# Kernel optimization log

Hardware: AMD Instinct MI355X
Metric: run time of the kernel (lower is better)

Reference implementation:

```python
import jax, jax.numpy as jnp
import numpy as np

B, IN, OUT, G, K = 8192, 2048, 2048, 5, 3
EPS = 1e-8


def b_spline_basis(x, grid, k=K):
    # x: [B, in], grid: [in, G]
    Gn = grid.shape[1]
    diff = x[:, :, None] - grid[None, :, :]                      # [B, in, G]
    basis = ((diff >= 0) & (diff < 1)).astype(x.dtype)           # order-0 indicator
    for order in range(1, k + 1):
        js = np.arange(Gn - order)
        i2 = np.minimum(js + order, Gn - 1)       # clamp of original OOB index
        i3 = np.minimum(js + order + 1, Gn - 1)   # clamp of original OOB index
        prev = basis
        # note: original uses (diff[:,:,j] - grid[:,j]) = x - 2*grid[:,j]; kept faithfully
        t1 = (diff[:, :, js] - grid[:, js]) / (grid[:, i2] - grid[:, js] + EPS) * prev[:, :, js]
        t2 = (grid[:, i3] - diff[:, :, js]) / (grid[:, i3] - grid[:, js + 1] + EPS) * prev[:, :, js + 1]
        basis = basis.at[:, :, js].set(t1 + t2)
    return basis


def setup_inputs() -> dict:
    key = jax.random.key(0)
    k1, k2, k3, k4, k5 = jax.random.split(key, 5)
    bound = 1.0 / np.sqrt(IN)
    x = jax.random.normal(k1, (B, IN), dtype=jnp.float32)
    base_weight = jax.random.uniform(k2, (OUT, IN), dtype=jnp.float32, minval=-bound, maxval=bound)
    base_bias = jax.random.uniform(k3, (OUT,), dtype=jnp.float32, minval=-bound, maxval=bound)
    spline_weight = jax.random.uniform(k4, (OUT, IN, G), dtype=jnp.float32, minval=-0.1, maxval=0.1)
    grid = jax.random.uniform(k5, (IN, G), dtype=jnp.float32, minval=-1.0, maxval=1.0)
    return {"x": x, "base_weight": base_weight, "base_bias": base_bias,
            "spline_weight": spline_weight, "grid": grid}


def reference(x, base_weight, base_bias, spline_weight, grid):
    base_output = x @ base_weight.T + base_bias                   # [B, out]
    spline_basis = b_spline_basis(x, grid, K)                     # [B, in, G]
    spline_output = jnp.einsum('big,oig->bo', spline_basis, spline_weight)
    return base_output + spline_output
```

## Files before the change

### kernel.cpp

```cpp
#include <hip/hip_runtime.h>
#include <hip/hip_bf16.h>

#define EPS 1e-8f

constexpr int B_   = 8192;
constexpr int IN_  = 2048;
constexpr int OUT_ = 2048;
constexpr int KA_  = IN_ * 6;
constexpr int NT_  = KA_ / 64;

typedef __bf16 bf16x8 __attribute__((ext_vector_type(8)));
typedef float  f32x4  __attribute__((ext_vector_type(4)));

__device__ __forceinline__ ushort f2bf(float f) {
    union { float f; uint u; } v; v.f = f;
    uint u = v.u;
    uint r = u + 0x7fffu + ((u >> 16) & 1u);
    return (ushort)(r >> 16);
}

__device__ __forceinline__ void gload16(const void* g, void* l) {
    __builtin_amdgcn_global_load_lds(
        (const __attribute__((address_space(1))) void*)g,
        (__attribute__((address_space(3))) void*)l,
        16, 0, 0);
}

__global__ __launch_bounds__(256) void stage_a(const float* __restrict__ x,
                                               const float* __restrict__ grid,
                                               ushort* __restrict__ A) {
    __shared__ __attribute__((aligned(16))) ushort pack[1536];
    const int tid = threadIdx.x;
    const int b0  = blockIdx.x * 16;
    const int i0  = blockIdx.y * 256;
    const int i   = i0 + tid;

    float g[5];
#pragma unroll
    for (int j = 0; j < 5; ++j) g[j] = grid[i * 5 + j];

    float r1[9], r2[9];
    {
        int t = 0;
#pragma unroll
        for (int o = 1; o <= 3; ++o) {
#pragma unroll
            for (int j = 0; j < 5 - o; ++j) {
                int i2 = min(j + o, 4);
                int i3 = min(j + o + 1, 4);
                r1[t] = 1.0f / (g[i2] - g[j] + EPS);
                r2[t] = 1.0f / (g[i3] - g[j + 1] + EPS);
                ++t;
            }
        }
    }

    for (int r = 0; r < 16; ++r) {
        const int b = b0 + r;
        float xv = x[(size_t)b * IN_ + i];
        float diff[5], bas[5];
#pragma unroll
        for (int j = 0; j < 5; ++j) {
            diff[j] = xv - g[j];
            bas[j]  = (diff[j] >= 0.0f && diff[j] < 1.0f) ? 1.0f : 0.0f;
        }
        int t = 0;
#pragma unroll
        for (int o = 1; o <= 3; ++o) {
            float nb[4];
#pragma unroll
            for (int j = 0; j < 5 - o; ++j) {
                int i3 = min(j + o + 1, 4);
                float t1 = (diff[j] - g[j]) * r1[t] * bas[j];
                float t2 = (g[i3] - diff[j]) * r2[t] * bas[j + 1];
                nb[j] = t1 + t2;
                ++t;
            }
#pragma unroll
            for (int j = 0; j < 5 - o; ++j) bas[j] = nb[j];
        }

        pack[tid * 6 + 0] = f2bf(xv);
#pragma unroll
        for (int j = 0; j < 5; ++j) pack[tid * 6 + 1 + j] = f2bf(bas[j]);
        __syncthreads();
        {
            const uint* ps = (const uint*)pack;
            uint* pd = (uint*)(A + (size_t)b * KA_ + (size_t)i0 * 6);
#pragma unroll
            for (int j = 0; j < 3; ++j) pd[tid + j * 256] = ps[tid + j * 256];
        }
        __syncthreads();
    }
}

__global__ __launch_bounds__(256) void stage_w(const float* __restrict__ bw,
                                               const float* __restrict__ sw,
                                               ushort* __restrict__ W) {
    __shared__ __attribute__((aligned(16))) float  ssh[1280];
    __shared__ __attribute__((aligned(16))) ushort wsh[1536];
    const int tid = threadIdx.x;
    const int o   = blockIdx.x;
    const int i0  = blockIdx.y * 256;

    const float* sp = sw + ((size_t)o * IN_ + i0) * 5;
    for (int j = tid; j < 1280; j += 256) ssh[j] = sp[j];
    float bwv = bw[(size_t)o * IN_ + i0 + tid];
    __syncthreads();

    wsh[tid * 6] = f2bf(bwv);
#pragma unroll
    for (int j = 0; j < 5; ++j) wsh[tid * 6 + 1 + j] = f2bf(ssh[tid * 5 + j]);
    __syncthreads();

    const uint* ps = (const uint*)wsh;
    uint* pd = (uint*)(W + (size_t)o * KA_ + (size_t)i0 * 6);
#pragma unroll
    for (int j = 0; j < 3; ++j) pd[tid + j * 256] = ps[tid + j * 256];
}

__global__ __launch_bounds__(512, 2) void gemm_kan8(const ushort* __restrict__ A,
                                                    const ushort* __restrict__ W,
                                                    const float* __restrict__ bias,
                                                    float* __restrict__ out) {
    __shared__ __attribute__((aligned(16))) char lds[2][2][32768];

    const int tid  = threadIdx.x;
    const int lane = tid & 63;
    const int wave = tid >> 6;
    const int wr   = wave >> 2;
    const int wc   = wave & 3;

    uint bid = blockIdx.x;
    uint swz = (bid & 7u) * 32u + (bid >> 3);
    const int bm = (int)(swz >> 3);
    const int bn = (int)(swz & 7u);

    const uint lhi16 = ((uint)lane >> 4) * 16u;
    const uint swx   = ((uint)lane & 7u) << 4;
    uint aro[8], wro[4];
#pragma unroll
    for (int m = 0; m < 8; ++m) aro[m] = (uint)(wr * 128 + m * 16 + (lane & 15)) * 128u;
#pragma unroll
    for (int n = 0; n < 4; ++n) wro[n] = (uint)(wc * 64 + n * 16 + (lane & 15)) * 128u;

    const uint srow0 = (uint)wave * 8u + ((uint)lane >> 3);
    const uint srow1 = srow0 + 64u;
    const uint gcol  = (((uint)lane & 7u) ^ (((uint)lane >> 3) & 7u)) * 8u;
    const ushort* pA0 = A + (size_t)bm * 256 * KA_ + (size_t)srow0 * KA_ + gcol;
    const ushort* pA1 = A + (size_t)bm * 256 * KA_ + (size_t)srow1 * KA_ + gcol;
    const ushort* pW0 = W + (size_t)bn * 256 * KA_ + (size_t)srow0 * KA_ + gcol;
    const ushort* pW1 = W + (size_t)bn * 256 * KA_ + (size_t)srow1 * KA_ + gcol;
    const uint c0off = (uint)wave * 1024u;
    const uint c1off = c0off + 8192u;

    f32x4 acc[8][4];
#pragma unroll
    for (int m = 0; m < 8; ++m)
#pragma unroll
        for (int n = 0; n < 4; ++n)
            acc[m][n] = (f32x4){0.f, 0.f, 0.f, 0.f};

#define DSR(base, ro, kh) (*(const bf16x8*)((base) + (ro) + (((kh) * 64u + lhi16) ^ swx)))

#define STAGE(s, mat, h, kk, PT0, PT1) do {                                   \
        uint kc_ = (uint)((kk) < NT_ ? (kk) : 0);                             \
        size_t go_ = (size_t)(h) * 128 * KA_ + (size_t)kc_ * 64;              \
        gload16(PT0 + go_, &lds[s][mat][(h) * 16384 + c0off]);                \
        gload16(PT1 + go_, &lds[s][mat][(h) * 16384 + c1off]);                \
    } while (0)

#define RDA(dst, base, mb) do {                                               \
        _Pragma("unroll") for (int m_ = 0; m_ < 4; ++m_) {                    \
            dst[m_][0] = DSR(base, aro[(mb) + m_], 0);                        \
            dst[m_][1] = DSR(base, aro[(mb) + m_], 1); } } while (0)

#define RDB(dst, base, nb) do {                                               \
        _Pragma("unroll") for (int n_ = 0; n_ < 2; ++n_) {                    \
            dst[n_][0] = DSR(base, wro[(nb) + n_], 0);                        \
            dst[n_][1] = DSR(base, wro[(nb) + n_], 1); } } while (0)

#define MIDBAR() do { __builtin_amdgcn_s_barrier();                           \
        asm volatile("s_waitcnt lgkmcnt(0)" ::: "memory");                    \
        __builtin_amdgcn_sched_barrier(0); } while (0)

#define MFMAQ(AF, BF, MB, NB) do {                                            \
        __builtin_amdgcn_s_setprio(1);                                        \
        _Pragma("unroll") for (int m_ = 0; m_ < 4; ++m_)                      \
        _Pragma("unroll") for (int n_ = 0; n_ < 2; ++n_) {                    \
            acc[(MB)+m_][(NB)+n_] = __builtin_amdgcn_mfma_f32_16x16x32_bf16(  \
                AF[m_][0], BF[n_][0], acc[(MB)+m_][(NB)+n_], 0, 0, 0);        \
            acc[(MB)+m_][(NB)+n_] = __builtin_amdgcn_mfma_f32_16x16x32_bf16(  \
                AF[m_][1], BF[n_][1], acc[(MB)+m_][(NB)+n_], 0, 0, 0);        \
        }                                                                     \
        __builtin_amdgcn_s_setprio(0);                                        \
        __builtin_amdgcn_s_barrier(); } while (0)

    const char* As0 = lds[0][0]; const char* Ws0 = lds[0][1];
    const char* As1 = lds[1][0]; const char* Ws1 = lds[1][1];

    STAGE(0, 0, 0, 0, pA0, pA1);
    STAGE(0, 0, 1, 0, pA0, pA1);
    STAGE(0, 1, 0, 0, pW0, pW1);
    STAGE(0, 1, 1, 0, pW0, pW1);
    STAGE(1, 1, 0, 1, pW0, pW1);
    STAGE(1, 1, 1, 1, pW0, pW1);
    asm volatile("s_waitcnt vmcnt(4)" ::: "memory");
    __builtin_amdgcn_s_barrier();

    bf16x8 a0[4][2], a1[4][2], b0[2][2], b1[2][2];

    for (int it = 0; it < NT_ / 2; ++it) {
        const int t1 = 2 * it + 1;
        RDA(a0, As0, 0); RDB(b0, Ws0, 0);
        STAGE(1, 0, 0, t1, pA0, pA1);
        MIDBAR(); MFMAQ(a0, b0, 0, 0);
        RDB(b1, Ws0, 2);
        STAGE(1, 0, 1, t1, pA0, pA1);
        MIDBAR(); MFMAQ(a0, b1, 0, 2);
        RDA(a1, As0, 4);
        STAGE(0, 1, 0, t1 + 1, pW0, pW1);
        MIDBAR(); MFMAQ(a1, b0, 4, 0);
        STAGE(0, 1, 1, t1 + 1, pW0, pW1);
        asm volatile("s_waitcnt vmcnt(4)" ::: "memory");
        MIDBAR(); MFMAQ(a1, b1, 4, 2);
        RDA(a0, As1, 0); RDB(b0, Ws1, 0);
        STAGE(0, 0, 0, t1 + 1, pA0, pA1);
        MIDBAR(); MFMAQ(a0, b0, 0, 0);
        RDB(b1, Ws1, 2);
        STAGE(0, 0, 1, t1 + 1, pA0, pA1);
        MIDBAR(); MFMAQ(a0, b1, 0, 2);
        RDA(a1, As1, 4);
        STAGE(1, 1, 0, t1 + 2, pW0, pW1);
        MIDBAR(); MFMAQ(a1, b0, 4, 0);
        STAGE(1, 1, 1, t1 + 2, pW0, pW1);
        asm volatile("s_waitcnt vmcnt(4)" ::: "memory");
        MIDBAR(); MFMAQ(a1, b1, 4, 2);
    }

    const int orow0 = bm * 256 + wr * 128;
    const int ocol0 = bn * 256 + wc * 64;
#pragma unroll
    for (int n = 0; n < 4; ++n) {
        int c = ocol0 + n * 16 + (lane & 15);
        float bv = bias[c];
#pragma unroll
        for (int m = 0; m < 8; ++m) {
            int r0 = orow0 + m * 16 + ((lane >> 4) << 2);
#pragma unroll
            for (int j = 0; j < 4; ++j)
                out[(size_t)(r0 + j) * OUT_ + c] = acc[m][n][j] + bv;
        }
    }
#undef DSR
#undef STAGE
#undef RDA
#undef RDB
#undef MIDBAR
#undef MFMAQ
}

__global__ __launch_bounds__(256) void kan_fallback(const float* __restrict__ x,
                                                    const float* __restrict__ bw,
                                                    const float* __restrict__ bb,
                                                    const float* __restrict__ sw,
                                                    const float* __restrict__ grid,
                                                    float* __restrict__ out) {
    __shared__ float ash[16 * 384];
    const int tid = threadIdx.x;
    const int o   = blockIdx.x * 256 + tid;
    const int b0  = blockIdx.y * 16;
    float acc[16];
#pragma unroll
    for (int r = 0; r < 16; ++r) acc[r] = 0.0f;

    for (int ic = 0; ic < IN_; ic += 64) {
        __syncthreads();
        for (int p = tid; p < 1024; p += 256) {
            int r = p >> 6, ii = p & 63;
            int i = ic + ii;
            float xv = x[(size_t)(b0 + r) * IN_ + i];
            float g[5];
#pragma unroll
            for (int j = 0; j < 5; ++j) g[j] = grid[i * 5 + j];
            float diff[5], bas[5];
#pragma unroll
            for (int j = 0; j < 5; ++j) {
                diff[j] = xv - g[j];
                bas[j]  = (diff[j] >= 0.0f && diff[j] < 1.0f) ? 1.0f : 0.0f;
            }
#pragma unroll
            for (int oo = 1; oo <= 3; ++oo) {
                float nb[4];
#pragma unroll
                for (int j = 0; j < 5 - oo; ++j) {
                    int i2 = min(j + oo, 4);
                    int i3 = min(j + oo + 1, 4);
                    nb[j] = (diff[j] - g[j]) / (g[i2] - g[j] + EPS) * bas[j]
                          + (g[i3] - diff[j]) / (g[i3] - g[j + 1] + EPS) * bas[j + 1];
                }
#pragma unroll
                for (int j = 0; j < 5 - oo; ++j) bas[j] = nb[j];
            }
            float* ap = &ash[r * 384 + ii * 6];
            ap[0] = xv;
#pragma unroll
            for (int j = 0; j < 5; ++j) ap[1 + j] = bas[j];
        }
        __syncthreads();
        for (int ii = 0; ii < 64; ++ii) {
            int i = ic + ii;
            float w0 = bw[(size_t)o * IN_ + i];
            const float* swp = sw + ((size_t)o * IN_ + i) * 5;
            float w1 = swp[0], w2 = swp[1], w3 = swp[2], w4 = swp[3], w5 = swp[4];
#pragma unroll
            for (int r = 0; r < 16; ++r) {
                const float* a = &ash[r * 384 + ii * 6];
                acc[r] += a[0] * w0 + a[1] * w1 + a[2] * w2
                        + a[3] * w3 + a[4] * w4 + a[5] * w5;
            }
        }
    }
    float bv = bb[o];
#pragma unroll
    for (int r = 0; r < 16; ++r)
        out[(size_t)(b0 + r) * OUT_ + o] = acc[r] + bv;
}

extern "C" void kernel_launch(void* const* d_in, const int* in_sizes, int n_in,
                              void* d_out, int out_size, void* d_ws, size_t ws_size,
                              hipStream_t stream) {
    (void)in_sizes; (void)n_in; (void)out_size;
    const float* x    = (const float*)d_in[0];
    const float* bw   = (const float*)d_in[1];
    const float* bb   = (const float*)d_in[2];
    const float* sw   = (const float*)d_in[3];
    const float* grid = (const float*)d_in[4];
    float* out = (float*)d_out;

    const size_t needA = (size_t)B_ * KA_ * sizeof(ushort);
    const size_t needW = (size_t)OUT_ * KA_ * sizeof(ushort);

    if (ws_size >= needA + needW) {
        ushort* A = (ushort*)d_ws;
        ushort* W = A + (size_t)B_ * KA_;
        stage_a<<<dim3(B_ / 16, IN_ / 256), 256, 0, stream>>>(x, grid, A);
        stage_w<<<dim3(OUT_, IN_ / 256), 256, 0, stream>>>(bw, sw, W);
        gemm_kan8<<<dim3(256), 512, 0, stream>>>(A, W, bb, out);
    } else {
        kan_fallback<<<dim3(OUT_ / 256, B_ / 16), 256, 0, stream>>>(x, bw, bb, sw, grid, out);
    }
}
```

Measured before the change: 422.4 us.

## Switch GEMM inner loop from 16x16x32 to 32x32x16 MFMA tiles

Replaces the 16x16x32 bf16 MFMA micro-tiles with 32x32x16 instructions. Each wave now covers its 128x64 output with 4x2 accumulator tiles of 16 floats, and the LDS read pattern and swizzle offsets are reworked to match the 32-row fragment layout. B fragments for all four k-subslices are loaded once per tile stage and A is reloaded per k-subslice. The epilogue is remapped to the 32x32 accumulator register layout. The intent is fewer LDS reads per flop and higher MFMA throughput, at the cost of different register pressure and a different LDS access pattern.

```diff
diff --git a/kernel.cpp b/kernel.cpp
--- a/kernel.cpp
+++ b/kernel.cpp
@@ -10,7 +10,7 @@
 constexpr int NT_  = KA_ / 64;
 
 typedef __bf16 bf16x8 __attribute__((ext_vector_type(8)));
-typedef float  f32x4  __attribute__((ext_vector_type(4)));
+typedef float  f32x16 __attribute__((ext_vector_type(16)));
 
 __device__ __forceinline__ ushort f2bf(float f) {
     union { float f; uint u; } v; v.f = f;
@@ -136,13 +136,13 @@
     const int bm = (int)(swz >> 3);
     const int bn = (int)(swz & 7u);
 
-    const uint lhi16 = ((uint)lane >> 4) * 16u;
-    const uint swx   = ((uint)lane & 7u) << 4;
-    uint aro[8], wro[4];
-#pragma unroll
-    for (int m = 0; m < 8; ++m) aro[m] = (uint)(wr * 128 + m * 16 + (lane & 15)) * 128u;
-#pragma unroll
-    for (int n = 0; n < 4; ++n) wro[n] = (uint)(wc * 64 + n * 16 + (lane & 15)) * 128u;
+    const uint l5   = ((uint)lane >> 5) * 16u;
+    const uint swx  = ((uint)lane & 7u) << 4;
+    uint aro[4], wro[2];
+#pragma unroll
+    for (int m = 0; m < 4; ++m) aro[m] = (uint)(wr * 128 + m * 32 + (lane & 31)) * 128u;
+#pragma unroll
+    for (int n = 0; n < 2; ++n) wro[n] = (uint)(wc * 64 + n * 32 + (lane & 31)) * 128u;
 
     const uint srow0 = (uint)wave * 8u + ((uint)lane >> 3);
     const uint srow1 = srow0 + 64u;
@@ -154,14 +154,14 @@
     const uint c0off = (uint)wave * 1024u;
     const uint c1off = c0off + 8192u;
 
-    f32x4 acc[8][4];
-#pragma unroll
-    for (int m = 0; m < 8; ++m)
-#pragma unroll
-        for (int n = 0; n < 4; ++n)
-            acc[m][n] = (f32x4){0.f, 0.f, 0.f, 0.f};
-
-#define DSR(base, ro, kh) (*(const bf16x8*)((base) + (ro) + (((kh) * 64u + lhi16) ^ swx)))
+    f32x16 acc[4][2];
+#pragma unroll
+    for (int m = 0; m < 4; ++m)
+#pragma unroll
+        for (int n = 0; n < 2; ++n)
+            acc[m][n] = (f32x16)(0.0f);
+
+#define DSR32(base, ro, kh) (*(const bf16x8*)((base) + (ro) + (((kh) * 32u + l5) ^ swx)))
 
 #define STAGE(s, mat, h, kk, PT0, PT1) do {                                   \
         uint kc_ = (uint)((kk) < NT_ ? (kk) : 0);                             \
@@ -170,31 +170,28 @@
         gload16(PT1 + go_, &lds[s][mat][(h) * 16384 + c1off]);                \
     } while (0)
 
-#define RDA(dst, base, mb) do {                                               \
-        _Pragma("unroll") for (int m_ = 0; m_ < 4; ++m_) {                    \
-            dst[m_][0] = DSR(base, aro[(mb) + m_], 0);                        \
-            dst[m_][1] = DSR(base, aro[(mb) + m_], 1); } } while (0)
-
-#define RDB(dst, base, nb) do {                                               \
-        _Pragma("unroll") for (int n_ = 0; n_ < 2; ++n_) {                    \
-            dst[n_][0] = DSR(base, wro[(nb) + n_], 0);                        \
-            dst[n_][1] = DSR(base, wro[(nb) + n_], 1); } } while (0)
+#define RDA32(dst, base, kh) do {                                             \
+        _Pragma("unroll") for (int m_ = 0; m_ < 4; ++m_)                      \
+            dst[m_] = DSR32(base, aro[m_], kh); } while (0)
+
+#define RDB32(dst, base) do {                                                 \
+        _Pragma("unroll") for (int n_ = 0; n_ < 2; ++n_)                      \
+        _Pragma("unroll") for (int k_ = 0; k_ < 4; ++k_)                      \
+            dst[n_][k_] = DSR32(base, wro[n_], k_); } while (0)
 
 #define MIDBAR() do { __builtin_amdgcn_s_barrier();                           \
         asm volatile("s_waitcnt lgkmcnt(0)" ::: "memory");                    \
         __builtin_amdgcn_sched_barrier(0); } while (0)
 
-#define MFMAQ(AF, BF, MB, NB) do {                                            \
+#define MFMA8(AF, BF, KH) do {                                                \
         __builtin_amdgcn_s_setprio(1);                                        \
         _Pragma("unroll") for (int m_ = 0; m_ < 4; ++m_)                      \
-        _Pragma("unroll") for (int n_ = 0; n_ < 2; ++n_) {                    \
-            acc[(MB)+m_][(NB)+n_] = __builtin_amdgcn_mfma_f32_16x16x32_bf16(  \
-                AF[m_][0], BF[n_][0], acc[(MB)+m_][(NB)+n_], 0, 0, 0);        \
-            acc[(MB)+m_][(NB)+n_] = __builtin_amdgcn_mfma_f32_16x16x32_bf16(  \
-                AF[m_][1], BF[n_][1], acc[(MB)+m_][(NB)+n_], 0, 0, 0);        \
-        }                                                                     \
-        __builtin_amdgcn_s_setprio(0);                                        \
-        __builtin_amdgcn_s_barrier(); } while (0)
+        _Pragma("unroll") for (int n_ = 0; n_ < 2; ++n_)                      \
+            acc[m_][n_] = __builtin_amdgcn_mfma_f32_32x32x16_bf16(            \
+                AF[m_], BF[n_][KH], acc[m_][n_], 0, 0, 0);                    \
+        __builtin_amdgcn_s_setprio(0); } while (0)
+
+#define ENDBAR() __builtin_amdgcn_s_barrier()
 
     const char* As0 = lds[0][0]; const char* Ws0 = lds[0][1];
     const char* As1 = lds[1][0]; const char* Ws1 = lds[1][1];
@@ -208,56 +205,61 @@
     asm volatile("s_waitcnt vmcnt(4)" ::: "memory");
     __builtin_amdgcn_s_barrier();
 
-    bf16x8 a0[4][2], a1[4][2], b0[2][2], b1[2][2];
+    bf16x8 a[4], b[2][4];
 
     for (int it = 0; it < NT_ / 2; ++it) {
         const int t1 = 2 * it + 1;
-        RDA(a0, As0, 0); RDB(b0, Ws0, 0);
+        RDA32(a, As0, 0); RDB32(b, Ws0);
         STAGE(1, 0, 0, t1, pA0, pA1);
-        MIDBAR(); MFMAQ(a0, b0, 0, 0);
-        RDB(b1, Ws0, 2);
+        MIDBAR(); MFMA8(a, b, 0); ENDBAR();
+        RDA32(a, As0, 1);
         STAGE(1, 0, 1, t1, pA0, pA1);
-        MIDBAR(); MFMAQ(a0, b1, 0, 2);
-        RDA(a1, As0, 4);
+        MIDBAR(); MFMA8(a, b, 1); ENDBAR();
+        RDA32(a, As0, 2);
         STAGE(0, 1, 0, t1 + 1, pW0, pW1);
-        MIDBAR(); MFMAQ(a1, b0, 4, 0);
+        MIDBAR(); MFMA8(a, b, 2); ENDBAR();
+        RDA32(a, As0, 3);
         STAGE(0, 1, 1, t1 + 1, pW0, pW1);
         asm volatile("s_waitcnt vmcnt(4)" ::: "memory");
-        MIDBAR(); MFMAQ(a1, b1, 4, 2);
-        RDA(a0, As1, 0); RDB(b0, Ws1, 0);
+        MIDBAR(); MFMA8(a, b, 3); ENDBAR();
+        RDA32(a, As1, 0); RDB32(b, Ws1);
         STAGE(0, 0, 0, t1 + 1, pA0, pA1);
-        MIDBAR(); MFMAQ(a0, b0, 0, 0);
-        RDB(b1, Ws1, 2);
+        MIDBAR(); MFMA8(a, b, 0); ENDBAR();
+        RDA32(a, As1, 1);
         STAGE(0, 0, 1, t1 + 1, pA0, pA1);
-        MIDBAR(); MFMAQ(a0, b1, 0, 2);
-        RDA(a1, As1, 4);
+        MIDBAR(); MFMA8(a, b, 1); ENDBAR();
+        RDA32(a, As1, 2);
         STAGE(1, 1, 0, t1 + 2, pW0, pW1);
-        MIDBAR(); MFMAQ(a1, b0, 4, 0);
+        MIDBAR(); MFMA8(a, b, 2); ENDBAR();
+        RDA32(a, As1, 3);
         STAGE(1, 1, 1, t1 + 2, pW0, pW1);
         asm volatile("s_waitcnt vmcnt(4)" ::: "memory");
-        MIDBAR(); MFMAQ(a1, b1, 4, 2);
-    }
-
-    const int orow0 = bm * 256 + wr * 128;
-    const int ocol0 = bn * 256 + wc * 64;
-#pragma unroll
-    for (int n = 0; n < 4; ++n) {
-        int c = ocol0 + n * 16 + (lane & 15);
+        MIDBAR(); MFMA8(a, b, 3); ENDBAR();
+    }
+
+    const int orow0 = bm * 256 + wr * 128 + ((lane >> 5) << 2);
+    const int ocol0 = bn * 256 + wc * 64 + (lane & 31);
+#pragma unroll
+    for (int n = 0; n < 2; ++n) {
+        int c = ocol0 + n * 32;
         float bv = bias[c];
 #pragma unroll
-        for (int m = 0; m < 8; ++m) {
-            int r0 = orow0 + m * 16 + ((lane >> 4) << 2);
-#pragma unroll
-            for (int j = 0; j < 4; ++j)
-                out[(size_t)(r0 + j) * OUT_ + c] = acc[m][n][j] + bv;
-        }
-    }
-#undef DSR
+        for (int m = 0; m < 4; ++m) {
+            int r0 = orow0 + m * 32;
+#pragma unroll
+            for (int reg = 0; reg < 16; ++reg) {
+                int r = r0 + (reg & 3) + ((reg >> 2) << 3);
+                out[(size_t)r * OUT_ + c] = acc[m][n][reg] + bv;
+            }
+        }
+    }
+#undef DSR32
 #undef STAGE
-#undef RDA
-#undef RDB
+#undef RDA32
+#undef RDB32
 #undef MIDBAR
-#undef MFMAQ
+#undef MFMA8
+#undef ENDBAR
 }
 
 __global__ __launch_bounds__(256) void kan_fallback(const float* __restrict__ x,
```

After: 451.8 us. 1.07x slower.

## Merge MFMA quarter-phases into half-phases with fewer barriers per K-tile

Applied to the files above, without the earlier changes.

Restructures the main GEMM loop so each wave loads all four B fragments at once and issues 32 MFMAs per phase instead of 16. This halves the number of block-wide barriers and lgkmcnt waits per K-tile. It also reorders MFMAs so the k-half-0 products for all 16 tiles run before the k-half-1 products, which spaces out dependent accumulator updates. The cost is more live B fragment registers and coarser interleaving of global-to-LDS staging with compute, which can affect register pressure and load/compute overlap.

```diff
diff --git a/kernel.cpp b/kernel.cpp
--- a/kernel.cpp
+++ b/kernel.cpp
@@ -175,26 +175,28 @@
             dst[m_][0] = DSR(base, aro[(mb) + m_], 0);                        \
             dst[m_][1] = DSR(base, aro[(mb) + m_], 1); } } while (0)
 
-#define RDB(dst, base, nb) do {                                               \
-        _Pragma("unroll") for (int n_ = 0; n_ < 2; ++n_) {                    \
-            dst[n_][0] = DSR(base, wro[(nb) + n_], 0);                        \
-            dst[n_][1] = DSR(base, wro[(nb) + n_], 1); } } while (0)
+#define RDB4(dst, base) do {                                                  \
+        _Pragma("unroll") for (int n_ = 0; n_ < 4; ++n_) {                    \
+            dst[n_][0] = DSR(base, wro[n_], 0);                               \
+            dst[n_][1] = DSR(base, wro[n_], 1); } } while (0)
 
 #define MIDBAR() do { __builtin_amdgcn_s_barrier();                           \
         asm volatile("s_waitcnt lgkmcnt(0)" ::: "memory");                    \
         __builtin_amdgcn_sched_barrier(0); } while (0)
 
-#define MFMAQ(AF, BF, MB, NB) do {                                            \
+#define MFMA32(AF, BF, MB) do {                                               \
         __builtin_amdgcn_s_setprio(1);                                        \
         _Pragma("unroll") for (int m_ = 0; m_ < 4; ++m_)                      \
-        _Pragma("unroll") for (int n_ = 0; n_ < 2; ++n_) {                    \
-            acc[(MB)+m_][(NB)+n_] = __builtin_amdgcn_mfma_f32_16x16x32_bf16(  \
-                AF[m_][0], BF[n_][0], acc[(MB)+m_][(NB)+n_], 0, 0, 0);        \
-            acc[(MB)+m_][(NB)+n_] = __builtin_amdgcn_mfma_f32_16x16x32_bf16(  \
-                AF[m_][1], BF[n_][1], acc[(MB)+m_][(NB)+n_], 0, 0, 0);        \
-        }                                                                     \
-        __builtin_amdgcn_s_setprio(0);                                        \
-        __builtin_amdgcn_s_barrier(); } while (0)
+        _Pragma("unroll") for (int n_ = 0; n_ < 4; ++n_)                      \
+            acc[(MB)+m_][n_] = __builtin_amdgcn_mfma_f32_16x16x32_bf16(       \
+                AF[m_][0], BF[n_][0], acc[(MB)+m_][n_], 0, 0, 0);             \
+        _Pragma("unroll") for (int m_ = 0; m_ < 4; ++m_)                      \
+        _Pragma("unroll") for (int n_ = 0; n_ < 4; ++n_)                      \
+            acc[(MB)+m_][n_] = __builtin_amdgcn_mfma_f32_16x16x32_bf16(       \
+                AF[m_][1], BF[n_][1], acc[(MB)+m_][n_], 0, 0, 0);             \
+        __builtin_amdgcn_s_setprio(0); } while (0)
+
+#define ENDBAR() __builtin_amdgcn_s_barrier()
 
     const char* As0 = lds[0][0]; const char* Ws0 = lds[0][1];
     const char* As1 = lds[1][0]; const char* Ws1 = lds[1][1];
@@ -208,34 +210,28 @@
     asm volatile("s_waitcnt vmcnt(4)" ::: "memory");
     __builtin_amdgcn_s_barrier();
 
-    bf16x8 a0[4][2], a1[4][2], b0[2][2], b1[2][2];
+    bf16x8 a0[4][2], a1[4][2], b[4][2];
 
     for (int it = 0; it < NT_ / 2; ++it) {
         const int t1 = 2 * it + 1;
-        RDA(a0, As0, 0); RDB(b0, Ws0, 0);
+        RDA(a0, As0, 0); RDB4(b, Ws0);
         STAGE(1, 0, 0, t1, pA0, pA1);
-        MIDBAR(); MFMAQ(a0, b0, 0, 0);
-        RDB(b1, Ws0, 2);
         STAGE(1, 0, 1, t1, pA0, pA1);
-        MIDBAR(); MFMAQ(a0, b1, 0, 2);
+        MIDBAR(); MFMA32(a0, b, 0); ENDBAR();
         RDA(a1, As0, 4);
         STAGE(0, 1, 0, t1 + 1, pW0, pW1);
-        MIDBAR(); MFMAQ(a1, b0, 4, 0);
         STAGE(0, 1, 1, t1 + 1, pW0, pW1);
         asm volatile("s_waitcnt vmcnt(4)" ::: "memory");
-        MIDBAR(); MFMAQ(a1, b1, 4, 2);
-        RDA(a0, As1, 0); RDB(b0, Ws1, 0);
+        MIDBAR(); MFMA32(a1, b, 4); ENDBAR();
+        RDA(a0, As1, 0); RDB4(b, Ws1);
         STAGE(0, 0, 0, t1 + 1, pA0, pA1);
-        MIDBAR(); MFMAQ(a0, b0, 0, 0);
-        RDB(b1, Ws1, 2);
         STAGE(0, 0, 1, t1 + 1, pA0, pA1);
-        MIDBAR(); MFMAQ(a0, b1, 0, 2);
+        MIDBAR(); MFMA32(a0, b, 0); ENDBAR();
         RDA(a1, As1, 4);
         STAGE(1, 1, 0, t1 + 2, pW0, pW1);
-        MIDBAR(); MFMAQ(a1, b0, 4, 0);
         STAGE(1, 1, 1, t1 + 2, pW0, pW1);
         asm volatile("s_waitcnt vmcnt(4)" ::: "memory");
-        MIDBAR(); MFMAQ(a1, b1, 4, 2);
+        MIDBAR(); MFMA32(a1, b, 4); ENDBAR();
     }
 
     const int orow0 = bm * 256 + wr * 128;
@@ -255,9 +251,10 @@
 #undef DSR
 #undef STAGE
 #undef RDA
-#undef RDB
+#undef RDB4
 #undef MIDBAR
-#undef MFMAQ
+#undef MFMA32
+#undef ENDBAR
 }
 
 __global__ __launch_bounds__(256) void kan_fallback(const float* __restrict__ x,
```

New measurement: 429.2 us. About the same (+1.6%).
